# Optimization experiments

Measured on AMD Instinct MI355X. Metric: run time of the kernel, lower is better.

The kernel has to match this reference:

```python
import jax, jax.numpy as jnp
import numpy as np


def _softsplat(inp, flow):
    # inp: [N,C,H,W], flow: [N,2,H,W] -> bilinear forward splat via 4 scatter-adds
    n, c, h, w = inp.shape
    hw = h * w
    yy, xx = jnp.meshgrid(jnp.arange(h, dtype=inp.dtype), jnp.arange(w, dtype=inp.dtype), indexing='ij')
    xx = xx[None] + flow[:, 0]  # [N,H,W] target x coords
    yy = yy[None] + flow[:, 1]  # [N,H,W] target y coords
    x0 = jnp.floor(xx); y0 = jnp.floor(yy)
    x1 = x0 + 1.0;      y1 = y0 + 1.0
    corners = (
        (x0, y0, (x1 - xx) * (y1 - yy)),
        (x1, y0, (xx - x0) * (y1 - yy)),
        (x0, y1, (x1 - xx) * (yy - y0)),
        (x1, y1, (xx - x0) * (yy - y0)),
    )
    batch_off = (jnp.arange(n, dtype=jnp.int32) * hw)[:, None, None]  # [N,1,1]
    vals_base = inp.transpose(1, 0, 2, 3)  # [C,N,H,W]
    out = jnp.zeros((c, n * hw), dtype=inp.dtype)
    for xi, yi, wgt in corners:  # fixed 4-way unroll
        xl = xi.astype(jnp.int32)
        yl = yi.astype(jnp.int32)
        valid = (xl >= 0) & (xl < w) & (yl >= 0) & (yl < h)
        lin = jnp.clip(yl, 0, h - 1) * w + jnp.clip(xl, 0, w - 1) + batch_off  # [N,H,W]
        wv = wgt * valid.astype(inp.dtype)  # [N,H,W]
        vals = (vals_base * wv[None]).reshape(c, -1)  # [C, N*H*W]
        out = out.at[:, lin.reshape(-1)].add(vals)
    return out.reshape(c, n, h, w).transpose(1, 0, 2, 3)


def setup_inputs() -> dict:
    key = jax.random.key(0)
    k1, k2, k3 = jax.random.split(key, 3)
    tenInput = jax.random.normal(k1, (4, 64, 256, 448), dtype=jnp.float32)
    tenFlow = jax.random.normal(k2, (4, 2, 256, 448), dtype=jnp.float32) * 4.0
    tenMetric = jax.random.normal(k3, (4, 1, 256, 448), dtype=jnp.float32)
    return {"tenInput": tenInput, "tenFlow": tenFlow, "tenMetric": tenMetric}


def reference(tenInput, tenFlow, tenMetric):
    # strType == 'softmax'
    metric = jnp.exp(tenMetric)  # [N,1,H,W]
    inp = jnp.concatenate([tenInput * metric, metric], axis=1)  # [N,C+1,H,W]
    out = _softsplat(inp, tenFlow)
    norm = out[:, -1:]
    norm = jnp.where(norm == 0.0, jnp.ones_like(norm), norm)
    return out[:, :-1] / norm
```

## Files before the change

kernel.cpp:

```cpp
#include <hip/hip_runtime.h>

#define NB 4
#define CH 64
#define HH 256
#define WW 448
constexpr int HW     = HH * WW;
constexpr int NPIX   = NB * HW;
constexpr int NROWS  = NB * HH;
constexpr int NTILE  = NPIX / 64;
constexpr int ROWCAP = 1536;
constexpr int FCAP   = 2 * ROWCAP;

constexpr size_t CNT_OFF  = 1024;
constexpr size_t OFF_OFF  = CNT_OFF + (size_t)NPIX;
constexpr size_t CE_OFF   = OFF_OFF + (size_t)NPIX;
constexpr size_t FE_OFF   = CE_OFF + (size_t)NROWS * ROWCAP * 4;
constexpr size_t TINP_OFF = FE_OFF + (size_t)NROWS * FCAP * 2;

__device__ __forceinline__ unsigned int bf16rne(float f) {
    unsigned int u = __float_as_uint(f);
    return (u + 0x7FFFu + ((u >> 16) & 1u)) >> 16;
}

__global__ __launch_bounds__(256) void pass_a(
    const float* __restrict__ inp, const float* __restrict__ flow,
    const float* __restrict__ metric,
    unsigned int* __restrict__ tinp, int* __restrict__ row_counts,
    int4* __restrict__ centries)
{
    __shared__ float tile[64][CH + 1];
    __shared__ float sfx[64], sfy[64], sm[64];
    __shared__ int whist[64], wbase[64];

    int b   = blockIdx.x;
    int blk = (b & 7) * (NTILE / 8) + (b >> 3);
    int nb    = blk / (HW / 64);
    int tpix0 = (blk - nb * (HW / 64)) * 64;
    int t = threadIdx.x;

    if (t < 64)        sfx[t]       = flow[(nb * 2 + 0) * HW + tpix0 + t];
    else if (t < 128)  sfy[t - 64]  = flow[(nb * 2 + 1) * HW + tpix0 + (t - 64)];
    else if (t < 192)  sm[t - 128]  = expf(metric[nb * HW + tpix0 + (t - 128)]);
    else               whist[t - 192] = 0;

    {
        int x4  = t & 15;
        int cc0 = t >> 4;
        const float* ipb = inp + (size_t)nb * CH * HW + tpix0 + x4 * 4;
        #pragma unroll
        for (int j = 0; j < 4; ++j) {
            int c = cc0 + j * 16;
            float4 v = *reinterpret_cast<const float4*>(ipb + (size_t)c * HW);
            tile[x4 * 4 + 0][c] = v.x;
            tile[x4 * 4 + 1][c] = v.y;
            tile[x4 * 4 + 2][c] = v.z;
            tile[x4 * 4 + 3][c] = v.w;
        }
    }
    __syncthreads();

    int y     = tpix0 / WW;
    int xbase = tpix0 - y * WW;

    bool emit = false;
    int  bin = -1, lrank = 0, rglob = -1, srcp = 0, x0c = 0;
    float wl = 0.0f, wr = 0.0f;

    if (t < 128) {
        int pl = t & 63, rsel = t >> 6;
        float fx = sfx[pl], fy = sfy[pl], m = sm[pl];
        float yy  = (float)y + fy;
        float y0f = floorf(yy);
        int   yr  = (int)y0f + rsel;
        float wyr = rsel ? (yy - y0f) : (1.0f - (yy - y0f));
        int   xq  = xbase + pl;
        float xx  = (float)xq + fx;
        float x0f = floorf(xx);
        int   x0  = (int)x0f;
        float wxf = xx - x0f;

        if (yr >= 0 && yr < HH && x0 >= -1 && x0 <= WW - 1) {
            emit = true;
            srcp = nb * HW + y * WW + xq;
            wl = (1.0f - wxf) * wyr * m;
            wr = wxf * wyr * m;
            if (x0 < 0)            { x0c = 0;      wl = wr;  wr = 0.0f; }
            else if (x0 == WW - 1) { x0c = WW - 2; wr = wl;  wl = 0.0f; }
            else                   { x0c = x0; }
            rglob = nb * HH + yr;
            bin = yr - (y - 30);
            if (bin >= 0 && bin < 64) lrank = atomicAdd(&whist[bin], 1);
            else bin = -1;
        }
    }
    __syncthreads();

    if (t < 64 && whist[t] > 0)
        wbase[t] = atomicAdd(&row_counts[nb * HH + (y - 30) + t], whist[t]);
    __syncthreads();

    if (emit) {
        int rank = (bin >= 0) ? (wbase[bin] + lrank)
                              : atomicAdd(&row_counts[rglob], 1);
        if (rank < ROWCAP)
            centries[(size_t)rglob * ROWCAP + rank] =
                make_int4(srcp, x0c, __float_as_int(wl), __float_as_int(wr));
    }

    int q  = t >> 2;
    int cb = (t & 3) * 16;
    unsigned int pk[8];
    #pragma unroll
    for (int j = 0; j < 8; ++j) {
        unsigned int lo = bf16rne(tile[q][cb + 2 * j]);
        unsigned int hi = bf16rne(tile[q][cb + 2 * j + 1]);
        pk[j] = lo | (hi << 16);
    }
    unsigned int* op = tinp + (size_t)(nb * HW + tpix0 + q) * 32 + (cb >> 1);
    *reinterpret_cast<uint4*>(op)     = make_uint4(pk[0], pk[1], pk[2], pk[3]);
    *reinterpret_cast<uint4*>(op + 4) = make_uint4(pk[4], pk[5], pk[6], pk[7]);
}

__global__ __launch_bounds__(256) void pass_c(
    const int* __restrict__ row_counts, const int4* __restrict__ centries,
    int* __restrict__ counts, int* __restrict__ offs, int2* __restrict__ fentries)
{
    __shared__ int4 ce[ROWCAP];
    __shared__ int hist[512];
    __shared__ int pstart[512];
    __shared__ int cur[WW];
    __shared__ int tmp[256];

    int r   = blockIdx.x;
    int tid = threadIdx.x;
    int nE  = row_counts[r];
    if (nE > ROWCAP) nE = ROWCAP;

    for (int e = tid; e < nE; e += 256) ce[e] = centries[(size_t)r * ROWCAP + e];
    for (int i = tid; i < 512; i += 256) hist[i] = 0;
    __syncthreads();

    for (int e = tid; e < nE; e += 256) {
        int x0 = ce[e].y;
        atomicAdd(&hist[x0], 1);
        atomicAdd(&hist[x0 + 1], 1);
    }
    __syncthreads();

    int a0 = hist[2 * tid], a1 = hist[2 * tid + 1];
    int s = a0 + a1;
    tmp[tid] = s;
    __syncthreads();
    int val = s;
    for (int d = 1; d < 256; d <<= 1) {
        int xv = (tid >= d) ? tmp[tid - d] : 0;
        __syncthreads();
        val += xv;
        tmp[tid] = val;
        __syncthreads();
    }
    int ex = val - s;
    pstart[2 * tid]     = ex;
    pstart[2 * tid + 1] = ex + a0;
    __syncthreads();

    int nbq = r / HH, yq = r - nbq * HH;
    size_t tb = (size_t)nbq * HW + (size_t)yq * WW;
    int rowbase = r * FCAP;
    for (int x = tid; x < WW; x += 256) {
        counts[tb + x] = hist[x];
        offs[tb + x]   = rowbase + pstart[x];
        cur[x] = pstart[x];
    }
    __syncthreads();

    for (int e = tid; e < nE; e += 256) {
        int4 en = ce[e];
        int x0 = en.y;
        int rkL = atomicAdd(&cur[x0], 1);
        int rkR = atomicAdd(&cur[x0 + 1], 1);
        fentries[rowbase + rkL] = make_int2(en.x, en.z);
        fentries[rowbase + rkR] = make_int2(en.x, en.w);
    }
}

__device__ __forceinline__ void bfma2(float& alo, float& ahi, float w, unsigned int u) {
    alo = fmaf(w, __uint_as_float(u << 16), alo);
    ahi = fmaf(w, __uint_as_float(u & 0xFFFF0000u), ahi);
}

__global__ __launch_bounds__(448) void gather_row(
    const uint4* __restrict__ tinp, const int* __restrict__ row_counts,
    const int* __restrict__ counts, const int* __restrict__ offs,
    const int2* __restrict__ fentries, float* __restrict__ out)
{
    __shared__ int2 eb[FCAP];

    int b = blockIdx.x;
    int r = (b & 7) * (NROWS / 8) + (b >> 3);
    int tid = threadIdx.x;

    int rowbase = r * FCAP;
    int tot = row_counts[r] * 2;
    if (tot > FCAP) tot = FCAP;
    for (int e = tid; e < tot; e += 448) eb[e] = fentries[rowbase + e];

    int nbq = r / HH, yq = r - nbq * HH;
    int t = nbq * HW + yq * WW + tid;
    int k  = counts[t];
    int mo = offs[t] - rowbase;
    __syncthreads();

    float ksum = 0.0f;
    for (int e = 0; e < k; ++e) ksum += __int_as_float(eb[mo + e].y);
    float rn = (ksum == 0.0f) ? 1.0f : 1.0f / ksum;

    size_t tbase = (size_t)nbq * CH * HW + (size_t)yq * WW + tid;

    #pragma unroll
    for (int g = 0; g < 4; ++g) {
        float a[16];
        #pragma unroll
        for (int j = 0; j < 16; ++j) a[j] = 0.0f;

        for (int e = 0; e < k; ++e) {
            int2 en = eb[mo + e];
            float w = __int_as_float(en.y);
            size_t bi = (size_t)en.x * 8 + g * 2;
            uint4 v0 = tinp[bi];
            uint4 v1 = tinp[bi + 1];
            bfma2(a[0],  a[1],  w, v0.x);
            bfma2(a[2],  a[3],  w, v0.y);
            bfma2(a[4],  a[5],  w, v0.z);
            bfma2(a[6],  a[7],  w, v0.w);
            bfma2(a[8],  a[9],  w, v1.x);
            bfma2(a[10], a[11], w, v1.y);
            bfma2(a[12], a[13], w, v1.z);
            bfma2(a[14], a[15], w, v1.w);
        }
        float* ob = out + tbase + (size_t)(g * 16) * HW;
        #pragma unroll
        for (int j = 0; j < 16; ++j)
            __builtin_nontemporal_store(a[j] * rn, ob + (size_t)j * HW);
    }
}

extern "C" void kernel_launch(void* const* d_in, const int* in_sizes, int n_in,
                              void* d_out, int out_size, void* d_ws, size_t ws_size,
                              hipStream_t stream) {
    const float* tenInput  = (const float*)d_in[0];
    const float* tenFlow   = (const float*)d_in[1];
    const float* tenMetric = (const float*)d_in[2];
    float* out = (float*)d_out;

    int*          row_counts = (int*)d_ws;
    int*          counts     = row_counts + CNT_OFF;
    int*          offs       = row_counts + OFF_OFF;
    int4*         centries   = (int4*)(row_counts + CE_OFF);
    int2*         fentries   = (int2*)(row_counts + FE_OFF);
    unsigned int* tinp       = (unsigned int*)(row_counts + TINP_OFF);

    hipMemsetAsync(row_counts, 0, NROWS * sizeof(int), stream);

    pass_a<<<NTILE, 256, 0, stream>>>(tenInput, tenFlow, tenMetric,
                                      tinp, row_counts, centries);
    pass_c<<<NROWS, 256, 0, stream>>>(row_counts, centries, counts, offs, fentries);
    gather_row<<<NROWS, 448, 0, stream>>>((const uint4*)tinp, row_counts,
                                          counts, offs, fentries, out);
}
```

Measured before the change: 282.6 us.

## Store each source once per x0 and share right-neighbour contributions via shuffles

Each source entry is now bucketed only under its left target column x0 and carries both left and right weights, so its bf16 feature vector is fetched once instead of twice. Each thread accumulates left (A) and right (B) partial sums, and the right-neighbour sums are passed to the next column with __shfl_up, plus shared memory at wavefront boundaries. This roughly halves gather loads and the entry count, at the cost of twice the accumulator registers, extra syncthreads per channel group, and dropping the unroll of the g loop.

```diff
diff --git a/kernel.cpp b/kernel.cpp
--- a/kernel.cpp
+++ b/kernel.cpp
@@ -9,13 +9,12 @@
 constexpr int NROWS  = NB * HH;
 constexpr int NTILE  = NPIX / 64;
 constexpr int ROWCAP = 1536;
-constexpr int FCAP   = 2 * ROWCAP;
 
 constexpr size_t CNT_OFF  = 1024;
 constexpr size_t OFF_OFF  = CNT_OFF + (size_t)NPIX;
 constexpr size_t CE_OFF   = OFF_OFF + (size_t)NPIX;
 constexpr size_t FE_OFF   = CE_OFF + (size_t)NROWS * ROWCAP * 4;
-constexpr size_t TINP_OFF = FE_OFF + (size_t)NROWS * FCAP * 2;
+constexpr size_t TINP_OFF = FE_OFF + (size_t)NROWS * ROWCAP * 4;
 
 __device__ __forceinline__ unsigned int bf16rne(float f) {
     unsigned int u = __float_as_uint(f);
@@ -123,7 +122,7 @@
 
 __global__ __launch_bounds__(256) void pass_c(
     const int* __restrict__ row_counts, const int4* __restrict__ centries,
-    int* __restrict__ counts, int* __restrict__ offs, int2* __restrict__ fentries)
+    int* __restrict__ counts, int* __restrict__ offs, int4* __restrict__ fentries)
 {
     __shared__ int4 ce[ROWCAP];
     __shared__ int hist[512];
@@ -140,11 +139,8 @@
     for (int i = tid; i < 512; i += 256) hist[i] = 0;
     __syncthreads();
 
-    for (int e = tid; e < nE; e += 256) {
-        int x0 = ce[e].y;
-        atomicAdd(&hist[x0], 1);
-        atomicAdd(&hist[x0 + 1], 1);
-    }
+    for (int e = tid; e < nE; e += 256)
+        atomicAdd(&hist[ce[e].y], 1);
     __syncthreads();
 
     int a0 = hist[2 * tid], a1 = hist[2 * tid + 1];
@@ -166,7 +162,7 @@
 
     int nbq = r / HH, yq = r - nbq * HH;
     size_t tb = (size_t)nbq * HW + (size_t)yq * WW;
-    int rowbase = r * FCAP;
+    int rowbase = r * ROWCAP;
     for (int x = tid; x < WW; x += 256) {
         counts[tb + x] = hist[x];
         offs[tb + x]   = rowbase + pstart[x];
@@ -176,11 +172,8 @@
 
     for (int e = tid; e < nE; e += 256) {
         int4 en = ce[e];
-        int x0 = en.y;
-        int rkL = atomicAdd(&cur[x0], 1);
-        int rkR = atomicAdd(&cur[x0 + 1], 1);
-        fentries[rowbase + rkL] = make_int2(en.x, en.z);
-        fentries[rowbase + rkR] = make_int2(en.x, en.w);
+        int s2 = atomicAdd(&cur[en.y], 1);
+        fentries[rowbase + s2] = make_int4(en.x, en.z, en.w, 0);
     }
 }
 
@@ -192,56 +185,78 @@
 __global__ __launch_bounds__(448) void gather_row(
     const uint4* __restrict__ tinp, const int* __restrict__ row_counts,
     const int* __restrict__ counts, const int* __restrict__ offs,
-    const int2* __restrict__ fentries, float* __restrict__ out)
+    const int4* __restrict__ fentries, float* __restrict__ out)
 {
-    __shared__ int2 eb[FCAP];
+    __shared__ int4  eb[ROWCAP];
+    __shared__ float hand[8];
+    __shared__ float handg[8][16];
 
     int b = blockIdx.x;
     int r = (b & 7) * (NROWS / 8) + (b >> 3);
-    int tid = threadIdx.x;
-
-    int rowbase = r * FCAP;
-    int tot = row_counts[r] * 2;
-    if (tot > FCAP) tot = FCAP;
-    for (int e = tid; e < tot; e += 448) eb[e] = fentries[rowbase + e];
+    int tid  = threadIdx.x;
+    int lane = tid & 63, wid = tid >> 6;
+
+    int rowbase = r * ROWCAP;
+    int nE = row_counts[r];
+    if (nE > ROWCAP) nE = ROWCAP;
+    for (int e = tid; e < nE; e += 448) eb[e] = fentries[rowbase + e];
 
     int nbq = r / HH, yq = r - nbq * HH;
-    int t = nbq * HW + yq * WW + tid;
+    int t  = nbq * HW + yq * WW + tid;
     int k  = counts[t];
     int mo = offs[t] - rowbase;
     __syncthreads();
 
-    float ksum = 0.0f;
-    for (int e = 0; e < k; ++e) ksum += __int_as_float(eb[mo + e].y);
-    float rn = (ksum == 0.0f) ? 1.0f : 1.0f / ksum;
+    float wsA = 0.0f, wsB = 0.0f;
+    for (int e = 0; e < k; ++e) {
+        wsA += __int_as_float(eb[mo + e].y);
+        wsB += __int_as_float(eb[mo + e].z);
+    }
+    if (lane == 63) hand[wid] = wsB;
+    __syncthreads();
+    float wsL = __shfl_up(wsB, 1);
+    if (lane == 0) wsL = (wid > 0) ? hand[wid - 1] : 0.0f;
+    float ws = wsA + wsL;
+    float rn = (ws == 0.0f) ? 1.0f : 1.0f / ws;
 
     size_t tbase = (size_t)nbq * CH * HW + (size_t)yq * WW + tid;
 
-    #pragma unroll
     for (int g = 0; g < 4; ++g) {
-        float a[16];
+        float A[16], B[16];
         #pragma unroll
-        for (int j = 0; j < 16; ++j) a[j] = 0.0f;
+        for (int j = 0; j < 16; ++j) { A[j] = 0.0f; B[j] = 0.0f; }
 
         for (int e = 0; e < k; ++e) {
-            int2 en = eb[mo + e];
-            float w = __int_as_float(en.y);
+            int4 en = eb[mo + e];
+            float wl = __int_as_float(en.y);
+            float wr = __int_as_float(en.z);
             size_t bi = (size_t)en.x * 8 + g * 2;
             uint4 v0 = tinp[bi];
             uint4 v1 = tinp[bi + 1];
-            bfma2(a[0],  a[1],  w, v0.x);
-            bfma2(a[2],  a[3],  w, v0.y);
-            bfma2(a[4],  a[5],  w, v0.z);
-            bfma2(a[6],  a[7],  w, v0.w);
-            bfma2(a[8],  a[9],  w, v1.x);
-            bfma2(a[10], a[11], w, v1.y);
-            bfma2(a[12], a[13], w, v1.z);
-            bfma2(a[14], a[15], w, v1.w);
-        }
+            bfma2(A[0],  A[1],  wl, v0.x);  bfma2(B[0],  B[1],  wr, v0.x);
+            bfma2(A[2],  A[3],  wl, v0.y);  bfma2(B[2],  B[3],  wr, v0.y);
+            bfma2(A[4],  A[5],  wl, v0.z);  bfma2(B[4],  B[5],  wr, v0.z);
+            bfma2(A[6],  A[7],  wl, v0.w);  bfma2(B[6],  B[7],  wr, v0.w);
+            bfma2(A[8],  A[9],  wl, v1.x);  bfma2(B[8],  B[9],  wr, v1.x);
+            bfma2(A[10], A[11], wl, v1.y);  bfma2(B[10], B[11], wr, v1.y);
+            bfma2(A[12], A[13], wl, v1.z);  bfma2(B[12], B[13], wr, v1.z);
+            bfma2(A[14], A[15], wl, v1.w);  bfma2(B[14], B[15], wr, v1.w);
+        }
+
+        if (lane == 63) {
+            #pragma unroll
+            for (int j = 0; j < 16; ++j) handg[wid][j] = B[j];
+        }
+        __syncthreads();
+
         float* ob = out + tbase + (size_t)(g * 16) * HW;
         #pragma unroll
-        for (int j = 0; j < 16; ++j)
-            __builtin_nontemporal_store(a[j] * rn, ob + (size_t)j * HW);
+        for (int j = 0; j < 16; ++j) {
+            float bl = __shfl_up(B[j], 1);
+            if (lane == 0) bl = (wid > 0) ? handg[wid - 1][j] : 0.0f;
+            __builtin_nontemporal_store((A[j] + bl) * rn, ob + (size_t)j * HW);
+        }
+        __syncthreads();
     }
 }
 
@@ -257,7 +272,7 @@
     int*          counts     = row_counts + CNT_OFF;
     int*          offs       = row_counts + OFF_OFF;
     int4*         centries   = (int4*)(row_counts + CE_OFF);
-    int2*         fentries   = (int2*)(row_counts + FE_OFF);
+    int4*         fentries   = (int4*)(row_counts + FE_OFF);
     unsigned int* tinp       = (unsigned int*)(row_counts + TINP_OFF);
 
     hipMemsetAsync(row_counts, 0, NROWS * sizeof(int), stream);
```

Result: no change. 281.5 us (-0.4%).
